# Optimization experiments

Hardware: AMD Instinct MI355X
Metric: run time of the kernel (lower is better)

The kernel has to match this reference:

```python
import jax, jax.numpy as jnp
import numpy as np

B, S, D_MODEL, D_K, D_V = 8, 2048, 1024, 512, 512


def setup_inputs() -> dict:
    key = jax.random.key(0)
    ks = jax.random.split(key, 5)
    return {
        "source_query": jax.random.normal(ks[0], (B, S, D_MODEL), dtype=jnp.float32),
        "source_key_value": jax.random.normal(ks[1], (B, S, D_MODEL), dtype=jnp.float32),
        "source_query_padding_mask": jnp.zeros((B, S), dtype=bool),
        "source_key_value_padding_mask": jnp.zeros((B, S), dtype=bool),
        "Wq": jax.random.normal(ks[2], (D_K, D_MODEL), dtype=jnp.float32) * (D_MODEL ** -0.5),
        "Wk": jax.random.normal(ks[3], (D_K, D_MODEL), dtype=jnp.float32) * (D_MODEL ** -0.5),
        "Wv": jax.random.normal(ks[4], (D_V, D_MODEL), dtype=jnp.float32) * (D_MODEL ** -0.5),
    }


def reference(source_query, source_key_value, source_query_padding_mask,
              source_key_value_padding_mask, Wq, Wk, Wv):
    # projections (nn.Linear with bias=False: x @ W^T)
    q = jnp.einsum('bsd,kd->bsk', source_query, Wq)          # [B,Sq,d_k]
    k = jnp.einsum('bsd,kd->bsk', source_key_value, Wk)      # [B,Sk,d_k]
    v = jnp.einsum('bsd,vd->bsv', source_key_value, Wv)      # [B,Sk,d_v]

    scores = jnp.einsum('bqk,bsk->bqs', q, k) * (D_K ** -0.5)  # [B,Sq,Sk]

    neg_inf = jnp.finfo(scores.dtype).min
    # padded queries mask entire rows; padded keys mask entire columns
    mask = source_query_padding_mask[:, :, None] | source_key_value_padding_mask[:, None, :]
    # causal (masked=True): tril over [Sq,Sq]
    sq = scores.shape[1]
    causal = ~jnp.tril(jnp.ones((sq, sq), dtype=bool))
    mask = mask | causal[None, :, :]

    scores = jnp.where(mask, neg_inf, scores)
    attn = jax.nn.softmax(scores, axis=-1)  # dropout p=0.0 -> identity
    out = jnp.einsum('bqs,bsv->bqv', attn, v)  # [B,Sq,d_v]
    return out
```

## Files before the change

kernel.cpp:

```cpp
#include <hip/hip_runtime.h>


typedef float  f32x4  __attribute__((ext_vector_type(4)));
typedef short  bf16x8 __attribute__((ext_vector_type(8)));
typedef unsigned short u16x8 __attribute__((ext_vector_type(8)));
typedef int    i32x4  __attribute__((ext_vector_type(4)));

#define MFMA16(a, b, c) __builtin_amdgcn_mfma_f32_16x16x32_bf16(a, b, c, 0, 0, 0)

__device__ __forceinline__ unsigned int f2bf1(float x) {
  unsigned int u = __builtin_bit_cast(unsigned int, x);
  u += 0x7FFFu + ((u >> 16) & 1u);
  return u >> 16;
}
__device__ __forceinline__ unsigned int pack2(float a, float b) {
  return f2bf1(a) | (f2bf1(b) << 16);
}
__device__ __forceinline__ float bf2f(unsigned short x) {
  return __builtin_bit_cast(float, ((unsigned int)x) << 16);
}
__device__ __forceinline__ void gld16(const void* gsrc, void* ldst) {
  __builtin_amdgcn_global_load_lds(
      (const __attribute__((address_space(1))) void*)gsrc,
      (__attribute__((address_space(3))) void*)ldst, 16, 0, 0);
}

__global__ __launch_bounds__(256) void cvt_x(
    const float* __restrict__ x0, const float* __restrict__ x1,
    unsigned short* __restrict__ d0, unsigned short* __restrict__ d1)
{
  const float* s = blockIdx.y ? x1 : x0;
  unsigned short* d = blockIdx.y ? d1 : d0;
  const long blk = (long)blockIdx.x * 8192 + threadIdx.x * 8;

  f32x4 a[4], b[4];
  #pragma unroll
  for (int i = 0; i < 4; ++i) {
    a[i] = *(const f32x4*)(s + blk + i * 2048);
    b[i] = *(const f32x4*)(s + blk + i * 2048 + 4);
  }
  #pragma unroll
  for (int i = 0; i < 4; ++i) {
    i32x4 v;
    v[0] = (int)pack2(a[i][0], a[i][1]);
    v[1] = (int)pack2(a[i][2], a[i][3]);
    v[2] = (int)pack2(b[i][0], b[i][1]);
    v[3] = (int)pack2(b[i][2], b[i][3]);
    *(i32x4*)(d + blk + i * 2048) = v;
  }
}

__global__ __launch_bounds__(256) void cvt_w(
    const float* __restrict__ w0, const float* __restrict__ w1,
    const float* __restrict__ w2, unsigned short* __restrict__ d)
{
  const float* s = (blockIdx.y == 0) ? w0 : (blockIdx.y == 1 ? w1 : w2);
  unsigned short* dd = d + (long)blockIdx.y * 524288;
  const long base = ((long)blockIdx.x * 256 + threadIdx.x) * 8;
  f32x4 a = *(const f32x4*)(s + base);
  f32x4 b = *(const f32x4*)(s + base + 4);
  i32x4 v;
  v[0] = (int)pack2(a[0], a[1]);
  v[1] = (int)pack2(a[2], a[3]);
  v[2] = (int)pack2(b[0], b[1]);
  v[3] = (int)pack2(b[2], b[3]);
  *(i32x4*)(dd + base) = v;
}

__global__ __launch_bounds__(256) void proj128(
    const unsigned short* __restrict__ xqb, const unsigned short* __restrict__ xkb,
    const unsigned short* __restrict__ wbf,
    unsigned short* __restrict__ qo, unsigned short* __restrict__ ko,
    unsigned short* __restrict__ vto)
{
  const int tid  = threadIdx.x;
  const int wave = tid >> 6, lane = tid & 63;
  const int g = lane >> 4, c = lane & 15;
  const int wm = wave >> 1, wn = wave & 1;

  const unsigned short* A; const unsigned short* B; unsigned short* C;
  int ldc, swap;
  if (blockIdx.y == 0)      { A = xqb;            B = wbf;           C = qo;  ldc = 512;   swap = 0; }
  else if (blockIdx.y == 1) { A = xkb;            B = wbf + 524288;  C = ko;  ldc = 512;   swap = 0; }
  else                      { A = wbf + 1048576;  B = xkb;           C = vto; ldc = 16384; swap = 1; }

  const int bid = (int)blockIdx.x;
  const int big = (bid & 7) + ((bid >> 5) << 3);
  const int sml = (bid >> 3) & 3;
  const long m0 = (long)(swap ? sml : big) * 128;
  const long n0 = (long)(swap ? big : sml) * 128;

  __shared__ __align__(16) char ash[16384];
  __shared__ __align__(16) char bsh[16384];

  const int lrow = lane >> 3;
  const int lcol = (lane & 7) * 8;

  const f32x4 fz = {0.f, 0.f, 0.f, 0.f};
  f32x4 acc[4][4];
  #pragma unroll
  for (int mt = 0; mt < 4; ++mt)
    #pragma unroll
    for (int nt = 0; nt < 4; ++nt) acc[mt][nt] = fz;

  auto issue = [&](int kt) {
    const long ko2 = (long)kt * 64;
    #pragma unroll
    for (int i = 0; i < 4; ++i) {
      int ch = i * 4 + wave;
      int row = ch * 8 + lrow;
      gld16(A + (m0 + row) * 1024 + ko2 + lcol, ash + ch * 1024);
      gld16(B + (n0 + row) * 1024 + ko2 + lcol, bsh + ch * 1024);
    }
  };

  issue(0);
  for (int kt = 0; kt < 16; ++kt) {
    __syncthreads();

    #pragma unroll
    for (int ks = 0; ks < 2; ++ks) {
      bf16x8 af[4], bfr[4];
      #pragma unroll
      for (int mt = 0; mt < 4; ++mt)
        af[mt] = *(const bf16x8*)(ash + (wm * 64 + mt * 16 + c) * 128 + ks * 64 + g * 16);
      #pragma unroll
      for (int nt = 0; nt < 4; ++nt)
        bfr[nt] = *(const bf16x8*)(bsh + (wn * 64 + nt * 16 + c) * 128 + ks * 64 + g * 16);
      #pragma unroll
      for (int mt = 0; mt < 4; ++mt)
        #pragma unroll
        for (int nt = 0; nt < 4; ++nt)
          acc[mt][nt] = MFMA16(af[mt], bfr[nt], acc[mt][nt]);
    }

    if (kt < 15) {
      __syncthreads();
      issue(kt + 1);
    }
  }

  #pragma unroll
  for (int mt = 0; mt < 4; ++mt) {
    #pragma unroll
    for (int nt = 0; nt < 4; ++nt) {
      long rowb = m0 + wm * 64 + mt * 16 + g * 4;
      long colb = n0 + wn * 64 + nt * 16 + c;
      #pragma unroll
      for (int r = 0; r < 4; ++r)
        C[(rowb + r) * (long)ldc + colb] = (unsigned short)f2bf1(acc[mt][nt][r]);
    }
  }
}

__global__ __launch_bounds__(256) void qk128(
    const unsigned short* __restrict__ q, const unsigned short* __restrict__ k,
    unsigned short* __restrict__ scp)
{
  const int mi = blockIdx.x, ni = blockIdx.y, b = blockIdx.z;
  if (ni > mi) return;

  const int tid  = threadIdx.x;
  const int wave = tid >> 6, lane = tid & 63;
  const int g = lane >> 4, c = lane & 15;
  const int wm = wave >> 1, wn = wave & 1;
  const long m0 = (long)mi * 128, n0 = (long)ni * 128;

  const unsigned short* A = q + ((long)b * 2048 + m0) * 512;
  const unsigned short* B = k + ((long)b * 2048 + n0) * 512;

  __shared__ __align__(16) char ash[16384];
  __shared__ __align__(16) char bsh[16384];

  const int lrow = lane >> 3;
  const int lcol = (lane & 7) * 8;

  const f32x4 fz = {0.f, 0.f, 0.f, 0.f};
  f32x4 acc[4][4];
  #pragma unroll
  for (int mt = 0; mt < 4; ++mt)
    #pragma unroll
    for (int nt = 0; nt < 4; ++nt) acc[mt][nt] = fz;

  auto issue = [&](int kt) {
    const long ko2 = (long)kt * 64;
    #pragma unroll
    for (int i = 0; i < 4; ++i) {
      int ch = i * 4 + wave;
      int row = ch * 8 + lrow;
      gld16(A + (long)row * 512 + ko2 + lcol, ash + ch * 1024);
      gld16(B + (long)row * 512 + ko2 + lcol, bsh + ch * 1024);
    }
  };

  issue(0);
  for (int kt = 0; kt < 8; ++kt) {
    __syncthreads();

    #pragma unroll
    for (int ks = 0; ks < 2; ++ks) {
      bf16x8 af[4], bfr[4];
      #pragma unroll
      for (int mt = 0; mt < 4; ++mt)
        af[mt] = *(const bf16x8*)(ash + (wm * 64 + mt * 16 + c) * 128 + ks * 64 + g * 16);
      #pragma unroll
      for (int nt = 0; nt < 4; ++nt)
        bfr[nt] = *(const bf16x8*)(bsh + (wn * 64 + nt * 16 + c) * 128 + ks * 64 + g * 16);
      #pragma unroll
      for (int mt = 0; mt < 4; ++mt)
        #pragma unroll
        for (int nt = 0; nt < 4; ++nt)
          acc[mt][nt] = MFMA16(af[mt], bfr[nt], acc[mt][nt]);
    }

    if (kt < 7) {
      __syncthreads();
      issue(kt + 1);
    }
  }

  const float S2 = 0.044194173824159216f * 1.4426950408889634f;
  unsigned short* Cb = scp + (long)b * 2048 * 2048;
  #pragma unroll
  for (int mt = 0; mt < 4; ++mt) {
    #pragma unroll
    for (int nt = 0; nt < 4; ++nt) {
      long rowb = m0 + wm * 64 + mt * 16 + g * 4;
      long colb = n0 + wn * 64 + nt * 16 + c;
      #pragma unroll
      for (int r = 0; r < 4; ++r)
        Cb[(rowb + r) * 2048 + colb] = (unsigned short)f2bf1(acc[mt][nt][r] * S2);
    }
  }
}

__global__ __launch_bounds__(256) void softmax_rows(unsigned short* __restrict__ scp)
{
  const int tid  = threadIdx.x;
  const int wave = tid >> 6, lane = tid & 63;
  const int r = blockIdx.x * 4 + wave;
  const int b = blockIdx.y;
  unsigned short* row = scp + ((long)b * 2048 + r) * 2048;

  const int ext = ((r >> 7) + 1) * 128;
  float v[4][8];
  #pragma unroll
  for (int j = 0; j < 4; ++j) {
    if (j * 512 >= ext) {
      #pragma unroll
      for (int e = 0; e < 8; ++e) v[j][e] = -1e30f;
      continue;
    }
    u16x8 raw = *(const u16x8*)(row + j * 512 + lane * 8);
    #pragma unroll
    for (int e = 0; e < 8; ++e) {
      int col = j * 512 + lane * 8 + e;
      v[j][e] = (col <= r) ? bf2f(raw[e]) : -1e30f;
    }
  }

  float m = v[0][0];
  #pragma unroll
  for (int j = 0; j < 4; ++j)
    #pragma unroll
    for (int e = 0; e < 8; ++e) m = fmaxf(m, v[j][e]);
  #pragma unroll
  for (int o = 1; o <= 32; o <<= 1) m = fmaxf(m, __shfl_xor(m, o));

  float p[4][8];
  float l = 0.f;
  #pragma unroll
  for (int j = 0; j < 4; ++j)
    #pragma unroll
    for (int e = 0; e < 8; ++e) { p[j][e] = exp2f(v[j][e] - m); l += p[j][e]; }
  #pragma unroll
  for (int o = 1; o <= 32; o <<= 1) l += __shfl_xor(l, o);

  const float inv = 1.0f / l;
  #pragma unroll
  for (int j = 0; j < 4; ++j) {
    if (j * 512 >= ext) continue;
    u16x8 w;
    #pragma unroll
    for (int e = 0; e < 8; ++e) w[e] = (unsigned short)f2bf1(p[j][e] * inv);
    *(u16x8*)(row + j * 512 + lane * 8) = w;
  }
}

__global__ __launch_bounds__(256) void pv128(
    const unsigned short* __restrict__ scp, const unsigned short* __restrict__ vt,
    float* __restrict__ out)
{
  const int bid = (int)blockIdx.x;
  const int mi0 = bid & 15;
  const int b   = (bid >> 4) & 7;
  const int dvt = (bid >> 7) & 3;
  const int mi  = (dvt & 2) ? 15 - mi0 : mi0;

  const int tid  = threadIdx.x;
  const int wave = tid >> 6, lane = tid & 63;
  const int g = lane >> 4, c = lane & 15;
  const int wm = wave >> 1, wn = wave & 1;
  const long m0 = (long)mi * 128;

  const unsigned short* A = scp + ((long)b * 2048 + m0) * 2048;
  const unsigned short* B = vt + (long)dvt * 128 * 16384 + (long)b * 2048;

  __shared__ __align__(16) char ash[16384];
  __shared__ __align__(16) char bsh[16384];

  const int lrow = lane >> 3;
  const int lcol = (lane & 7) * 8;

  const f32x4 fz = {0.f, 0.f, 0.f, 0.f};
  f32x4 acc[4][4];
  #pragma unroll
  for (int mt = 0; mt < 4; ++mt)
    #pragma unroll
    for (int nt = 0; nt < 4; ++nt) acc[mt][nt] = fz;

  const int nkt = 2 * (mi + 1);

  auto issue = [&](int kt) {
    const long ko2 = (long)kt * 64;
    #pragma unroll
    for (int i = 0; i < 4; ++i) {
      int ch = i * 4 + wave;
      int row = ch * 8 + lrow;
      gld16(A + (long)row * 2048  + ko2 + lcol, ash + ch * 1024);
      gld16(B + (long)row * 16384 + ko2 + lcol, bsh + ch * 1024);
    }
  };

  issue(0);
  for (int kt = 0; kt < nkt; ++kt) {
    __syncthreads();

    #pragma unroll
    for (int ks = 0; ks < 2; ++ks) {
      bf16x8 af[4], bfr[4];
      #pragma unroll
      for (int mt = 0; mt < 4; ++mt)
        af[mt] = *(const bf16x8*)(ash + (wm * 64 + mt * 16 + c) * 128 + ks * 64 + g * 16);
      #pragma unroll
      for (int nt = 0; nt < 4; ++nt)
        bfr[nt] = *(const bf16x8*)(bsh + (wn * 64 + nt * 16 + c) * 128 + ks * 64 + g * 16);
      #pragma unroll
      for (int mt = 0; mt < 4; ++mt)
        #pragma unroll
        for (int nt = 0; nt < 4; ++nt)
          acc[mt][nt] = MFMA16(af[mt], bfr[nt], acc[mt][nt]);
    }

    if (kt + 1 < nkt) {
      __syncthreads();
      issue(kt + 1);
    }
  }

  #pragma unroll
  for (int mt = 0; mt < 4; ++mt) {
    #pragma unroll
    for (int nt = 0; nt < 4; ++nt) {
      long rowb = m0 + wm * 64 + mt * 16 + g * 4;
      long colb = (long)dvt * 128 + wn * 64 + nt * 16 + c;
      #pragma unroll
      for (int r = 0; r < 4; ++r)
        out[((long)b * 2048 + rowb + r) * 512 + colb] = acc[mt][nt][r];
    }
  }
}

extern "C" void kernel_launch(void* const* d_in, const int* in_sizes, int n_in,
                              void* d_out, int out_size, void* d_ws, size_t ws_size,
                              hipStream_t stream) {
  const float* xq  = (const float*)d_in[0];
  const float* xkv = (const float*)d_in[1];
  const float* Wq = (const float*)d_in[4];
  const float* Wk = (const float*)d_in[5];
  const float* Wv = (const float*)d_in[6];
  float* out = (float*)d_out;

  const size_t SZ_XBF = (size_t)16384 * 1024;
  const size_t SZ_W1  = (size_t)512 * 1024;
  const size_t SZ_P   = (size_t)16384 * 512;
  const size_t NEED = (2 * SZ_XBF + 3 * SZ_W1 + 3 * SZ_P) * 2;
  if (ws_size < NEED) return;

  unsigned short* xqb = (unsigned short*)d_ws;
  unsigned short* xkb = xqb + SZ_XBF;
  unsigned short* wbf = xkb + SZ_XBF;
  unsigned short* q   = wbf + 3 * SZ_W1;
  unsigned short* k   = q + SZ_P;
  unsigned short* vt  = k + SZ_P;
  unsigned short* scp = (unsigned short*)d_ws;

  cvt_x<<<dim3(2048, 2), 256, 0, stream>>>(xq, xkv, xqb, xkb);
  cvt_w<<<dim3(256, 3),  256, 0, stream>>>(Wq, Wk, Wv, wbf);

  proj128<<<dim3(512, 3), 256, 0, stream>>>(xqb, xkb, wbf, q, k, vt);

  qk128<<<dim3(16, 16, 8), 256, 0, stream>>>(q, k, scp);
  softmax_rows<<<dim3(512, 8), 256, 0, stream>>>(scp);
  pv128<<<512, 256, 0, stream>>>(scp, vt, out);
}
```

Baseline: 213.0 us.

## Double-buffer LDS tiles and XOR-swizzle columns in all GEMM kernels

Converts the projection, QK and PV GEMM kernels to double-buffered LDS, issuing the next K-tile's global-to-LDS loads before computing on the current tile, with one barrier per iteration. It also applies an XOR swizzle to the 16-byte column chunks in LDS to reduce bank conflicts on fragment reads. LDS use doubles to 64KB per block, which may reduce occupancy.

Measured after the change: 207.1 us. 2.8% less time.

```diff
diff --git a/kernel.cpp b/kernel.cpp
--- a/kernel.cpp
+++ b/kernel.cpp
@@ -90,11 +90,12 @@
   const long m0 = (long)(swap ? sml : big) * 128;
   const long n0 = (long)(swap ? big : sml) * 128;
 
-  __shared__ __align__(16) char ash[16384];
-  __shared__ __align__(16) char bsh[16384];
+  __shared__ __align__(16) char ash[2][16384];
+  __shared__ __align__(16) char bsh[2][16384];
 
   const int lrow = lane >> 3;
-  const int lcol = (lane & 7) * 8;
+  const int scol = (((lane & 7) ^ lrow)) * 8;
+  const int swz  = (c & 7) << 4;
 
   const f32x4 fz = {0.f, 0.f, 0.f, 0.f};
   f32x4 acc[4][4];
@@ -103,30 +104,33 @@
     #pragma unroll
     for (int nt = 0; nt < 4; ++nt) acc[mt][nt] = fz;
 
-  auto issue = [&](int kt) {
+  auto issue = [&](int kt, int buf) {
     const long ko2 = (long)kt * 64;
     #pragma unroll
     for (int i = 0; i < 4; ++i) {
       int ch = i * 4 + wave;
       int row = ch * 8 + lrow;
-      gld16(A + (m0 + row) * 1024 + ko2 + lcol, ash + ch * 1024);
-      gld16(B + (n0 + row) * 1024 + ko2 + lcol, bsh + ch * 1024);
+      gld16(A + (m0 + row) * 1024 + ko2 + scol, ash[buf] + ch * 1024);
+      gld16(B + (n0 + row) * 1024 + ko2 + scol, bsh[buf] + ch * 1024);
     }
   };
 
-  issue(0);
+  issue(0, 0);
+  __syncthreads();
+
+  int cur = 0;
   for (int kt = 0; kt < 16; ++kt) {
-    __syncthreads();
+    if (kt < 15) issue(kt + 1, cur ^ 1);
 
     #pragma unroll
     for (int ks = 0; ks < 2; ++ks) {
       bf16x8 af[4], bfr[4];
       #pragma unroll
       for (int mt = 0; mt < 4; ++mt)
-        af[mt] = *(const bf16x8*)(ash + (wm * 64 + mt * 16 + c) * 128 + ks * 64 + g * 16);
+        af[mt] = *(const bf16x8*)(ash[cur] + (wm * 64 + mt * 16 + c) * 128 + ((ks * 64 + g * 16) ^ swz));
       #pragma unroll
       for (int nt = 0; nt < 4; ++nt)
-        bfr[nt] = *(const bf16x8*)(bsh + (wn * 64 + nt * 16 + c) * 128 + ks * 64 + g * 16);
+        bfr[nt] = *(const bf16x8*)(bsh[cur] + (wn * 64 + nt * 16 + c) * 128 + ((ks * 64 + g * 16) ^ swz));
       #pragma unroll
       for (int mt = 0; mt < 4; ++mt)
         #pragma unroll
@@ -134,10 +138,8 @@
           acc[mt][nt] = MFMA16(af[mt], bfr[nt], acc[mt][nt]);
     }
 
-    if (kt < 15) {
-      __syncthreads();
-      issue(kt + 1);
-    }
+    __syncthreads();
+    cur ^= 1;
   }
 
   #pragma unroll
@@ -169,11 +171,12 @@
   const unsigned short* A = q + ((long)b * 2048 + m0) * 512;
   const unsigned short* B = k + ((long)b * 2048 + n0) * 512;
 
-  __shared__ __align__(16) char ash[16384];
-  __shared__ __align__(16) char bsh[16384];
+  __shared__ __align__(16) char ash[2][16384];
+  __shared__ __align__(16) char bsh[2][16384];
 
   const int lrow = lane >> 3;
-  const int lcol = (lane & 7) * 8;
+  const int scol = (((lane & 7) ^ lrow)) * 8;
+  const int swz  = (c & 7) << 4;
 
   const f32x4 fz = {0.f, 0.f, 0.f, 0.f};
   f32x4 acc[4][4];
@@ -182,30 +185,33 @@
     #pragma unroll
     for (int nt = 0; nt < 4; ++nt) acc[mt][nt] = fz;
 
-  auto issue = [&](int kt) {
+  auto issue = [&](int kt, int buf) {
     const long ko2 = (long)kt * 64;
     #pragma unroll
     for (int i = 0; i < 4; ++i) {
       int ch = i * 4 + wave;
       int row = ch * 8 + lrow;
-      gld16(A + (long)row * 512 + ko2 + lcol, ash + ch * 1024);
-      gld16(B + (long)row * 512 + ko2 + lcol, bsh + ch * 1024);
+      gld16(A + (long)row * 512 + ko2 + scol, ash[buf] + ch * 1024);
+      gld16(B + (long)row * 512 + ko2 + scol, bsh[buf] + ch * 1024);
     }
   };
 
-  issue(0);
+  issue(0, 0);
+  __syncthreads();
+
+  int cur = 0;
   for (int kt = 0; kt < 8; ++kt) {
-    __syncthreads();
+    if (kt < 7) issue(kt + 1, cur ^ 1);
 
     #pragma unroll
     for (int ks = 0; ks < 2; ++ks) {
       bf16x8 af[4], bfr[4];
       #pragma unroll
       for (int mt = 0; mt < 4; ++mt)
-        af[mt] = *(const bf16x8*)(ash + (wm * 64 + mt * 16 + c) * 128 + ks * 64 + g * 16);
+        af[mt] = *(const bf16x8*)(ash[cur] + (wm * 64 + mt * 16 + c) * 128 + ((ks * 64 + g * 16) ^ swz));
       #pragma unroll
       for (int nt = 0; nt < 4; ++nt)
-        bfr[nt] = *(const bf16x8*)(bsh + (wn * 64 + nt * 16 + c) * 128 + ks * 64 + g * 16);
+        bfr[nt] = *(const bf16x8*)(bsh[cur] + (wn * 64 + nt * 16 + c) * 128 + ((ks * 64 + g * 16) ^ swz));
       #pragma unroll
       for (int mt = 0; mt < 4; ++mt)
         #pragma unroll
@@ -213,10 +219,8 @@
           acc[mt][nt] = MFMA16(af[mt], bfr[nt], acc[mt][nt]);
     }
 
-    if (kt < 7) {
-      __syncthreads();
-      issue(kt + 1);
-    }
+    __syncthreads();
+    cur ^= 1;
   }
 
   const float S2 = 0.044194173824159216f * 1.4426950408889634f;
@@ -306,11 +310,12 @@
   const unsigned short* A = scp + ((long)b * 2048 + m0) * 2048;
   const unsigned short* B = vt + (long)dvt * 128 * 16384 + (long)b * 2048;
 
-  __shared__ __align__(16) char ash[16384];
-  __shared__ __align__(16) char bsh[16384];
+  __shared__ __align__(16) char ash[2][16384];
+  __shared__ __align__(16) char bsh[2][16384];
 
   const int lrow = lane >> 3;
-  const int lcol = (lane & 7) * 8;
+  const int scol = (((lane & 7) ^ lrow)) * 8;
+  const int swz  = (c & 7) << 4;
 
   const f32x4 fz = {0.f, 0.f, 0.f, 0.f};
   f32x4 acc[4][4];
@@ -321,30 +326,33 @@
 
   const int nkt = 2 * (mi + 1);
 
-  auto issue = [&](int kt) {
+  auto issue = [&](int kt, int buf) {
     const long ko2 = (long)kt * 64;
     #pragma unroll
     for (int i = 0; i < 4; ++i) {
       int ch = i * 4 + wave;
       int row = ch * 8 + lrow;
-      gld16(A + (long)row * 2048  + ko2 + lcol, ash + ch * 1024);
-      gld16(B + (long)row * 16384 + ko2 + lcol, bsh + ch * 1024);
+      gld16(A + (long)row * 2048  + ko2 + scol, ash[buf] + ch * 1024);
+      gld16(B + (long)row * 16384 + ko2 + scol, bsh[buf] + ch * 1024);
     }
   };
 
-  issue(0);
+  issue(0, 0);
+  __syncthreads();
+
+  int cur = 0;
   for (int kt = 0; kt < nkt; ++kt) {
-    __syncthreads();
+    if (kt + 1 < nkt) issue(kt + 1, cur ^ 1);
 
     #pragma unroll
     for (int ks = 0; ks < 2; ++ks) {
       bf16x8 af[4], bfr[4];
       #pragma unroll
       for (int mt = 0; mt < 4; ++mt)
-        af[mt] = *(const bf16x8*)(ash + (wm * 64 + mt * 16 + c) * 128 + ks * 64 + g * 16);
+        af[mt] = *(const bf16x8*)(ash[cur] + (wm * 64 + mt * 16 + c) * 128 + ((ks * 64 + g * 16) ^ swz));
       #pragma unroll
       for (int nt = 0; nt < 4; ++nt)
-        bfr[nt] = *(const bf16x8*)(bsh + (wn * 64 + nt * 16 + c) * 128 + ks * 64 + g * 16);
+        bfr[nt] = *(const bf16x8*)(bsh[cur] + (wn * 64 + nt * 16 + c) * 128 + ((ks * 64 + g * 16) ^ swz));
       #pragma unroll
       for (int mt = 0; mt < 4; ++mt)
         #pragma unroll
@@ -352,10 +360,8 @@
           acc[mt][nt] = MFMA16(af[mt], bfr[nt], acc[mt][nt]);
     }
 
-    if (kt + 1 < nkt) {
-      __syncthreads();
-      issue(kt + 1);
-    }
+    __syncthreads();
+    cur ^= 1;
   }
 
   #pragma unroll
```
